# Performance work log

Hardware: AMD Instinct MI355X
Metric: run time of the kernel (lower is better)

Reference implementation:

```python
import jax, jax.numpy as jnp
import numpy as np

NUM_CLASSES = 26
IGNORE_LABEL = 0
LAMBDA_SMOOTH = 1.0
EPSILON = 1e-05
# static indices of valid (non-ignored) classes
_VALID = np.array([c for c in range(NUM_CLASSES) if c != IGNORE_LABEL])


def setup_inputs() -> dict:
    key = jax.random.key(0)
    k1, k2, k3 = jax.random.split(key, 3)
    B, D, H, W = 1, 160, 192, 224
    fixed_label_map = jax.random.randint(k1, (B, D, H, W), 0, NUM_CLASSES, dtype=jnp.int32)
    warped_moving_label_map = jax.random.randint(k2, (B, D, H, W), 0, NUM_CLASSES, dtype=jnp.int32)
    vector_field = jax.random.normal(k3, (B, 3, D, H, W), dtype=jnp.float32)
    return {
        'fixed_label_map': fixed_label_map,
        'warped_moving_label_map': warped_moving_label_map,
        'vector_field': vector_field,
    }


def _soft_dice(fixed, moving):
    # Equivalent to one-hot expansion + sum over (B,D,H,W), but computed
    # directly from integer labels via histogram counts (single pass).
    f = fixed.reshape(-1)
    m = moving.reshape(-1)
    fixed_vol = jnp.bincount(f, length=NUM_CLASSES).astype(jnp.float32)
    moving_vol = jnp.bincount(m, length=NUM_CLASSES).astype(jnp.float32)
    # intersection[c] = #{voxels: f==c and m==c}
    inter = jnp.bincount(f, weights=(f == m).astype(jnp.float32), length=NUM_CLASSES)
    dice = (2.0 * inter + EPSILON) / (fixed_vol + moving_vol + EPSILON)
    return 1.0 - dice[_VALID].mean()


def _diffusion(vf):
    # vf: [B, 3, D, H, W]
    dz = vf[:, :, 1:, :, :] - vf[:, :, :-1, :, :]
    dy = vf[:, :, :, 1:, :] - vf[:, :, :, :-1, :]
    dx = vf[:, :, :, :, 1:] - vf[:, :, :, :, :-1]
    return (jnp.mean(dz * dz) + jnp.mean(dy * dy) + jnp.mean(dx * dx)) / 3.0


def reference(fixed_label_map, warped_moving_label_map, vector_field):
    similarity_loss = _soft_dice(fixed_label_map, warped_moving_label_map)
    smoothness_loss = _diffusion(vector_field)
    total_loss = similarity_loss + LAMBDA_SMOOTH * smoothness_loss
    return (total_loss, similarity_loss, smoothness_loss)
```

## Files before the change

### kernel.cpp

```cpp
#include <hip/hip_runtime.h>


namespace {
constexpr int NC    = 26;
constexpr int Dd    = 160, Hh = 192, Ww = 224;
constexpr int W4    = Ww / 4;
constexpr int PL4   = Hh * W4;
constexpr int N4L   = Dd * Hh * Ww / 4;
constexpr int JSTRIDE = 33;
constexpr int NBINS   = NC * JSTRIDE;
constexpr int HIST_BLOCKS = 840;
constexpr int HT          = HIST_BLOCKS * 256;
constexpr int SLAB    = 6;
constexpr int SLABS   = Hh / SLAB;
constexpr int SGRPS   = SLABS / 4;
constexpr int DCH     = 5;
constexpr int DCHUNKS = Dd / DCH;
constexpr int DIFF_BLOCKS = 3 * DCHUNKS * SGRPS;
constexpr int GRP         = 8;
constexpr int DIFF_GRPS   = DIFF_BLOCKS / GRP;
constexpr int HIST_GRPS   = HIST_BLOCKS / GRP;
constexpr int PAIRED_GRPS = 2 * DIFF_GRPS;
constexpr int FUSED_BLOCKS = DIFF_BLOCKS + HIST_BLOCKS;
}

__global__ void init_ws_kernel(unsigned int* __restrict__ joint,
                               double* __restrict__ sums) {
    int i = blockIdx.x * blockDim.x + threadIdx.x;
    if (i < NBINS) joint[i] = 0u;
    if (i < 3)     sums[i]  = 0.0;
}

__device__ __forceinline__ void hist_path(
        int hb,
        const int4* __restrict__ f4,
        const int4* __restrict__ m4,
        unsigned int* __restrict__ gj) {
    __shared__ unsigned int h[NBINS];
    for (int i = threadIdx.x; i < NBINS; i += 256) h[i] = 0u;
    __syncthreads();

    const int g = hb * 256 + threadIdx.x;
    int4 a0 = f4[g];
    int4 a1 = f4[g + HT];
    int4 a2 = f4[g + 2 * HT];
    int4 a3 = f4[g + 3 * HT];
    int4 a4 = f4[g + 4 * HT];
    int4 a5 = f4[g + 5 * HT];
    int4 a6 = f4[g + 6 * HT];
    int4 a7 = f4[g + 7 * HT];
    int4 b0 = m4[g];
    int4 b1 = m4[g + HT];
    int4 b2 = m4[g + 2 * HT];
    int4 b3 = m4[g + 3 * HT];
    int4 b4 = m4[g + 4 * HT];
    int4 b5 = m4[g + 5 * HT];
    int4 b6 = m4[g + 6 * HT];
    int4 b7 = m4[g + 7 * HT];

#define JACC(A, B)                                   \
    atomicAdd(&h[(A).x * JSTRIDE + (B).x], 1u);      \
    atomicAdd(&h[(A).y * JSTRIDE + (B).y], 1u);      \
    atomicAdd(&h[(A).z * JSTRIDE + (B).z], 1u);      \
    atomicAdd(&h[(A).w * JSTRIDE + (B).w], 1u);
    JACC(a0, b0) JACC(a1, b1) JACC(a2, b2) JACC(a3, b3)
    JACC(a4, b4) JACC(a5, b5) JACC(a6, b6) JACC(a7, b7)
#undef JACC

    __syncthreads();
    for (int i = threadIdx.x; i < NBINS; i += 256) {
        unsigned int v = h[i];
        if (v) atomicAdd(&gj[i], v);
    }
}

__device__ __forceinline__ void diff_path(
        int db,
        const float4* __restrict__ v4,
        double* __restrict__ gs) {
    const int lane = threadIdx.x & 63;
    const int wid  = threadIdx.x >> 6;
    const int c      = db / (DCHUNKS * SGRPS);
    const int rem    = db % (DCHUNKS * SGRPS);
    const int dchunk = rem / SGRPS;
    const int sgrp   = rem % SGRPS;
    const int slab   = sgrp * 4 + wid;
    const int h0     = slab * SLAB;
    const int d0     = dchunk * DCH;
    const bool al    = (lane < W4);
    const bool hv    = (h0 + SLAB < Hh);
    const int  l     = al ? lane : (W4 - 1);

    size_t cur = ((size_t)(c * Dd + d0) * Hh + h0) * W4 + l;

    float4 p0 = v4[cur];
    float4 p1 = v4[cur + W4];
    float4 p2 = v4[cur + 2 * W4];
    float4 p3 = v4[cur + 3 * W4];
    float4 p4 = v4[cur + 4 * W4];
    float4 p5 = v4[cur + 5 * W4];

    float sx = 0.f, sy = 0.f, sz = 0.f;
    const int haloOff = (hv ? SLAB : SLAB - 1) * W4;

    for (int k = 0; k < DCH; ++k) {
        const int d = d0 + k;
        const bool dzv = (d < Dd - 1);
        float4 hl = v4[cur + haloOff];
        float4 n0 = p0, n1 = p1, n2 = p2, n3 = p3, n4 = p4, n5 = p5;
        if (dzv) {
            const size_t nb = cur + PL4;
            n0 = v4[nb];
            n1 = v4[nb + W4];
            n2 = v4[nb + 2 * W4];
            n3 = v4[nb + 3 * W4];
            n4 = v4[nb + 4 * W4];
            n5 = v4[nb + 5 * W4];
        }

#define DX(P)                                                                  \
        {                                                                      \
            float d1 = (P).y - (P).x, d2 = (P).z - (P).y, d3 = (P).w - (P).z;  \
            sx += d1 * d1 + d2 * d2 + d3 * d3;                                 \
            float nx = __shfl_down((P).x, 1);                                  \
            float d4 = nx - (P).w;                                             \
            sx += (lane < W4 - 1) ? d4 * d4 : 0.f;                             \
        }
        DX(p0) DX(p1) DX(p2) DX(p3) DX(p4) DX(p5)
#undef DX
#define DY(A, B)                                                               \
        {                                                                      \
            float e0 = (B).x - (A).x, e1 = (B).y - (A).y;                      \
            float e2 = (B).z - (A).z, e3 = (B).w - (A).w;                      \
            sy += e0 * e0 + e1 * e1 + e2 * e2 + e3 * e3;                       \
        }
        DY(p0, p1) DY(p1, p2) DY(p2, p3) DY(p3, p4) DY(p4, p5)
        if (hv) DY(p5, hl)
#undef DY
        if (dzv) {
#define DZ(A, B)                                                               \
            {                                                                  \
                float e0 = (B).x - (A).x, e1 = (B).y - (A).y;                  \
                float e2 = (B).z - (A).z, e3 = (B).w - (A).w;                  \
                sz += e0 * e0 + e1 * e1 + e2 * e2 + e3 * e3;                   \
            }
            DZ(p0, n0) DZ(p1, n1) DZ(p2, n2) DZ(p3, n3) DZ(p4, n4) DZ(p5, n5)
#undef DZ
        }
        p0 = n0; p1 = n1; p2 = n2; p3 = n3; p4 = n4; p5 = n5;
        cur += PL4;
    }

    if (!al) { sx = 0.f; sy = 0.f; sz = 0.f; }

    #pragma unroll
    for (int off = 32; off > 0; off >>= 1) {
        sx += __shfl_down(sx, off);
        sy += __shfl_down(sy, off);
        sz += __shfl_down(sz, off);
    }
    __shared__ float px[4], py[4], pz[4];
    if (lane == 0) { px[wid] = sx; py[wid] = sy; pz[wid] = sz; }
    __syncthreads();
    if (threadIdx.x == 0) {
        atomicAdd(&gs[0], (double)(px[0] + px[1] + px[2] + px[3]));
        atomicAdd(&gs[1], (double)(py[0] + py[1] + py[2] + py[3]));
        atomicAdd(&gs[2], (double)(pz[0] + pz[1] + pz[2] + pz[3]));
    }
}

__global__ __launch_bounds__(256, 3) void fused_kernel(
        const int4* __restrict__ f4,
        const int4* __restrict__ m4,
        unsigned int* __restrict__ gj,
        const float4* __restrict__ v4,
        double* __restrict__ gs) {
    const int grp = blockIdx.x >> 3;
    const int t   = blockIdx.x & 7;
    if (grp < PAIRED_GRPS) {
        const int idx = (grp >> 1) * GRP + t;
        if (grp & 1) hist_path(idx, f4, m4, gj);
        else         diff_path(idx, v4, gs);
    } else {
        hist_path(DIFF_BLOCKS + (grp - PAIRED_GRPS) * GRP + t, f4, m4, gj);
    }
}

__global__ void finalize_kernel(const unsigned int* __restrict__ gj,
                                const double* __restrict__ gs,
                                float* __restrict__ out) {
    int lane = threadIdx.x & 63;
    float term = 0.f;
    if (lane >= 1 && lane < NC) {
        float fv = 0.f, mv = 0.f;
        #pragma unroll
        for (int m = 0; m < NC; ++m) fv += (float)gj[lane * JSTRIDE + m];
        #pragma unroll
        for (int f = 0; f < NC; ++f) mv += (float)gj[f * JSTRIDE + lane];
        float iv = (float)gj[lane * JSTRIDE + lane];
        term = (2.f * iv + 1e-5f) / (fv + mv + 1e-5f);
    }
    #pragma unroll
    for (int off = 32; off > 0; off >>= 1) term += __shfl_down(term, off);
    if (threadIdx.x == 0 && blockIdx.x == 0) {
        float sim = 1.f - term * (1.f / 25.f);
        double mdx = gs[0] / ((double)3 * Dd * Hh * (Ww - 1));
        double mdy = gs[1] / ((double)3 * Dd * (Hh - 1) * Ww);
        double mdz = gs[2] / ((double)3 * (Dd - 1) * Hh * Ww);
        float smooth = (float)((mdx + mdy + mdz) / 3.0);
        out[0] = sim + smooth;
        out[1] = sim;
        out[2] = smooth;
    }
}

extern "C" void kernel_launch(void* const* d_in, const int* in_sizes, int n_in,
                              void* d_out, int out_size, void* d_ws, size_t ws_size,
                              hipStream_t stream) {
    const int*   fl = (const int*)d_in[0];
    const int*   ml = (const int*)d_in[1];
    const float* vf = (const float*)d_in[2];
    float* out = (float*)d_out;

    unsigned int* joint = (unsigned int*)d_ws;
    double*       sums  = (double*)((char*)d_ws + 3584);

    init_ws_kernel<<<1, 1024, 0, stream>>>(joint, sums);
    fused_kernel<<<FUSED_BLOCKS, 256, 0, stream>>>(
        (const int4*)fl, (const int4*)ml, joint, (const float4*)vf, sums);
    finalize_kernel<<<1, 64, 0, stream>>>(joint, sums, out);
}
```

Measured before the change: 178.2 us.

## Shrink diffusion depth chunks, unroll planes, and interleave two diff blocks per histogram block

The diffusion path now handles 2 depth planes per block instead of 5. Its loop becomes straight-line code that loads both planes plus the next plane up front, which more than doubles the number of diffusion blocks. The block schedule changes from alternating diff and histogram groups to a two-diff, one-histogram pattern, with the leftover diff groups placed at the end. The launch-bounds occupancy hint rises from 3 to 4 blocks per CU. The aim is more memory-level parallelism and better latency hiding, at the cost of re-reading more boundary planes from the vector field and possibly more register pressure.

```diff
diff --git a/kernel.cpp b/kernel.cpp
--- a/kernel.cpp
+++ b/kernel.cpp
@@ -14,13 +14,12 @@
 constexpr int SLAB    = 6;
 constexpr int SLABS   = Hh / SLAB;
 constexpr int SGRPS   = SLABS / 4;
-constexpr int DCH     = 5;
+constexpr int DCH     = 2;
 constexpr int DCHUNKS = Dd / DCH;
 constexpr int DIFF_BLOCKS = 3 * DCHUNKS * SGRPS;
-constexpr int GRP         = 8;
-constexpr int DIFF_GRPS   = DIFF_BLOCKS / GRP;
-constexpr int HIST_GRPS   = HIST_BLOCKS / GRP;
-constexpr int PAIRED_GRPS = 2 * DIFF_GRPS;
+constexpr int GRP       = 8;
+constexpr int TRIPLES   = HIST_BLOCKS / GRP;
+constexpr int PAT_GRPS  = 3 * TRIPLES;
 constexpr int FUSED_BLOCKS = DIFF_BLOCKS + HIST_BLOCKS;
 }
 
@@ -90,66 +89,74 @@
     const bool al    = (lane < W4);
     const bool hv    = (h0 + SLAB < Hh);
     const int  l     = al ? lane : (W4 - 1);
-
-    size_t cur = ((size_t)(c * Dd + d0) * Hh + h0) * W4 + l;
-
-    float4 p0 = v4[cur];
-    float4 p1 = v4[cur + W4];
-    float4 p2 = v4[cur + 2 * W4];
-    float4 p3 = v4[cur + 3 * W4];
-    float4 p4 = v4[cur + 4 * W4];
-    float4 p5 = v4[cur + 5 * W4];
+    const bool dz1   = (d0 + 1 < Dd - 1);
+
+    const size_t base = ((size_t)(c * Dd + d0) * Hh + h0) * W4 + l;
+    const int haloOff = (hv ? SLAB : SLAB - 1) * W4;
+
+    float4 a0 = v4[base];
+    float4 a1 = v4[base + W4];
+    float4 a2 = v4[base + 2 * W4];
+    float4 a3 = v4[base + 3 * W4];
+    float4 a4 = v4[base + 4 * W4];
+    float4 a5 = v4[base + 5 * W4];
+    float4 hA = v4[base + haloOff];
+    const size_t bb = base + PL4;
+    float4 b0 = v4[bb];
+    float4 b1 = v4[bb + W4];
+    float4 b2 = v4[bb + 2 * W4];
+    float4 b3 = v4[bb + 3 * W4];
+    float4 b4 = v4[bb + 4 * W4];
+    float4 b5 = v4[bb + 5 * W4];
+    float4 hB = v4[bb + haloOff];
+    float4 q0, q1, q2, q3, q4, q5;
+    if (dz1) {
+        const size_t cc = bb + PL4;
+        q0 = v4[cc];
+        q1 = v4[cc + W4];
+        q2 = v4[cc + 2 * W4];
+        q3 = v4[cc + 3 * W4];
+        q4 = v4[cc + 4 * W4];
+        q5 = v4[cc + 5 * W4];
+    } else {
+        q0 = b0; q1 = b1; q2 = b2; q3 = b3; q4 = b4; q5 = b5;
+    }
 
     float sx = 0.f, sy = 0.f, sz = 0.f;
-    const int haloOff = (hv ? SLAB : SLAB - 1) * W4;
-
-    for (int k = 0; k < DCH; ++k) {
-        const int d = d0 + k;
-        const bool dzv = (d < Dd - 1);
-        float4 hl = v4[cur + haloOff];
-        float4 n0 = p0, n1 = p1, n2 = p2, n3 = p3, n4 = p4, n5 = p5;
-        if (dzv) {
-            const size_t nb = cur + PL4;
-            n0 = v4[nb];
-            n1 = v4[nb + W4];
-            n2 = v4[nb + 2 * W4];
-            n3 = v4[nb + 3 * W4];
-            n4 = v4[nb + 4 * W4];
-            n5 = v4[nb + 5 * W4];
-        }
 
 #define DX(P)                                                                  \
-        {                                                                      \
-            float d1 = (P).y - (P).x, d2 = (P).z - (P).y, d3 = (P).w - (P).z;  \
-            sx += d1 * d1 + d2 * d2 + d3 * d3;                                 \
-            float nx = __shfl_down((P).x, 1);                                  \
-            float d4 = nx - (P).w;                                             \
-            sx += (lane < W4 - 1) ? d4 * d4 : 0.f;                             \
-        }
-        DX(p0) DX(p1) DX(p2) DX(p3) DX(p4) DX(p5)
+    {                                                                          \
+        float d1 = (P).y - (P).x, d2 = (P).z - (P).y, d3 = (P).w - (P).z;      \
+        sx += d1 * d1 + d2 * d2 + d3 * d3;                                     \
+        float nx = __shfl_down((P).x, 1);                                      \
+        float d4 = nx - (P).w;                                                 \
+        sx += (lane < W4 - 1) ? d4 * d4 : 0.f;                                 \
+    }
+#define DY(A, B)                                                               \
+    {                                                                          \
+        float e0 = (B).x - (A).x, e1 = (B).y - (A).y;                          \
+        float e2 = (B).z - (A).z, e3 = (B).w - (A).w;                          \
+        sy += e0 * e0 + e1 * e1 + e2 * e2 + e3 * e3;                           \
+    }
+#define DZ(A, B)                                                               \
+    {                                                                          \
+        float e0 = (B).x - (A).x, e1 = (B).y - (A).y;                          \
+        float e2 = (B).z - (A).z, e3 = (B).w - (A).w;                          \
+        sz += e0 * e0 + e1 * e1 + e2 * e2 + e3 * e3;                           \
+    }
+    DX(a0) DX(a1) DX(a2) DX(a3) DX(a4) DX(a5)
+    DY(a0, a1) DY(a1, a2) DY(a2, a3) DY(a3, a4) DY(a4, a5)
+    if (hv) DY(a5, hA)
+    DZ(a0, b0) DZ(a1, b1) DZ(a2, b2) DZ(a3, b3) DZ(a4, b4) DZ(a5, b5)
+    DX(b0) DX(b1) DX(b2) DX(b3) DX(b4) DX(b5)
+    DY(b0, b1) DY(b1, b2) DY(b2, b3) DY(b3, b4) DY(b4, b5)
+    if (hv) DY(b5, hB)
+    if (dz1) {
+        DZ(b0, q0) DZ(b1, q1) DZ(b2, q2) DZ(b3, q3) DZ(b4, q4) DZ(b5, q5)
+    }
 #undef DX
-#define DY(A, B)                                                               \
-        {                                                                      \
-            float e0 = (B).x - (A).x, e1 = (B).y - (A).y;                      \
-            float e2 = (B).z - (A).z, e3 = (B).w - (A).w;                      \
-            sy += e0 * e0 + e1 * e1 + e2 * e2 + e3 * e3;                       \
-        }
-        DY(p0, p1) DY(p1, p2) DY(p2, p3) DY(p3, p4) DY(p4, p5)
-        if (hv) DY(p5, hl)
 #undef DY
-        if (dzv) {
-#define DZ(A, B)                                                               \
-            {                                                                  \
-                float e0 = (B).x - (A).x, e1 = (B).y - (A).y;                  \
-                float e2 = (B).z - (A).z, e3 = (B).w - (A).w;                  \
-                sz += e0 * e0 + e1 * e1 + e2 * e2 + e3 * e3;                   \
-            }
-            DZ(p0, n0) DZ(p1, n1) DZ(p2, n2) DZ(p3, n3) DZ(p4, n4) DZ(p5, n5)
 #undef DZ
-        }
-        p0 = n0; p1 = n1; p2 = n2; p3 = n3; p4 = n4; p5 = n5;
-        cur += PL4;
-    }
 
     if (!al) { sx = 0.f; sy = 0.f; sz = 0.f; }
 
@@ -169,7 +176,7 @@
     }
 }
 
-__global__ __launch_bounds__(256, 3) void fused_kernel(
+__global__ __launch_bounds__(256, 4) void fused_kernel(
         const int4* __restrict__ f4,
         const int4* __restrict__ m4,
         unsigned int* __restrict__ gj,
@@ -177,12 +184,13 @@
         double* __restrict__ gs) {
     const int grp = blockIdx.x >> 3;
     const int t   = blockIdx.x & 7;
-    if (grp < PAIRED_GRPS) {
-        const int idx = (grp >> 1) * GRP + t;
-        if (grp & 1) hist_path(idx, f4, m4, gj);
-        else         diff_path(idx, v4, gs);
+    if (grp < PAT_GRPS) {
+        const int tri = grp / 3;
+        const int r   = grp - tri * 3;
+        if (r == 2) hist_path(tri * GRP + t, f4, m4, gj);
+        else        diff_path((tri * 2 + r) * GRP + t, v4, gs);
     } else {
-        hist_path(DIFF_BLOCKS + (grp - PAIRED_GRPS) * GRP + t, f4, m4, gj);
+        diff_path((2 * TRIPLES + (grp - PAT_GRPS)) * GRP + t, v4, gs);
     }
 }
 
```

New measurement: 202.0 us. 1.13x slower.
